# Optimization experiments

Hardware: AMD Instinct MI355X
Metric: run time of the kernel (lower is better)

Reference implementation:

```python
import jax, jax.numpy as jnp
import numpy as np
from jax import lax

B, C, L, G = 2048, 9605, 20, 50
ALPHA, ALPHA1, ALPHA2, ALPHA3, ALPHA_OTHER = 0.5, 0.05, 2.0, 10.0, 0.5
NEG_INF = jnp.float32(-1e30)


def setup_inputs() -> dict:
    k0, k1, k2, k3 = jax.random.split(jax.random.key(0), 4)
    x = jax.random.normal(k0, (B, C), jnp.float32)
    # sparse multi-label targets (~10 positives/row) so at most ~1 whitelist group is active,
    # matching the original code's assert len(gt_whitelist_index) == 1
    y = (jax.random.uniform(k1, (B, C)) < 0.001).astype(jnp.int32)
    y_neg = (jax.random.uniform(k2, (B, C)) < 0.001).astype(jnp.int32)
    # L disjoint whitelist groups of G classes each (from mapping_dict in the original)
    idx = jax.random.permutation(k3, C)[: L * G].reshape(L, G)
    group_mask = jnp.zeros((L, C), bool).at[jnp.arange(L)[:, None], idx].set(True)
    return {"x": x, "y": y, "y_neg": y_neg, "group_mask": group_mask}


def _rank_loss(x1, x2, margin):
    # our_rank_loss: sigmoid(alpha3*(x2-x1+margin)), scaled by alpha2 when positive
    d = x2 - x1 + margin
    s = jax.nn.sigmoid(ALPHA3 * d)
    return jnp.where(d > 0, ALPHA2 * s, s)


def reference(x, y, y_neg, group_mask):
    xs = jax.nn.sigmoid(x)  # [B, C]
    gmf = group_mask.astype(jnp.float32)  # [L, C]

    # per-row max score inside each whitelist group -> [B, L]
    # lax.map over the L (=20) groups keeps peak memory at one [B, C] temp per step
    group_max = lax.map(
        lambda m: jnp.max(jnp.where(m, xs, NEG_INF), axis=-1), group_mask
    ).T  # [B, L]

    # find_gt_whitelist: group k active iff sum(y[group_k]) > 0
    active = jnp.einsum("bc,lc->bl", y.astype(jnp.float32), gmf) > 0
    active_neg = jnp.einsum("bc,lc->bl", y_neg.astype(jnp.float32), gmf) > 0
    has_gt = jnp.any(active, axis=-1)  # [B]
    g = jnp.argmax(active, axis=-1)  # first active group (original asserts exactly one)

    # top_k_thres = max(11th largest sigmoid score, alpha_other) in both branches
    thres = jnp.maximum(lax.top_k(xs, 11)[0][:, 10], ALPHA_OTHER)  # [B]

    # max over union of all whitelist classes (wl_indices)
    union_max = jnp.max(jnp.where(jnp.any(group_mask, 0)[None, :], xs, NEG_INF), -1)

    gt_max = jnp.take_along_axis(group_max, g[:, None], axis=1)[:, 0]  # [B]
    # incorrect_max: max(0, max over groups != g); incorrect_neg: max(0, max over neg-active groups)
    excl = jnp.where(jnp.arange(L)[None, :] == g[:, None], NEG_INF, group_max)
    incorrect_max = jnp.maximum(jnp.max(excl, -1), 0.0)
    incorrect_neg = jnp.maximum(jnp.max(jnp.where(active_neg, group_max, 0.0), -1), 0.0)

    # branch A: no gt whitelist group active
    case_a = (1 - ALPHA) * _rank_loss(thres, union_max, ALPHA1) + ALPHA * _rank_loss(
        thres, incorrect_neg, ALPHA1
    )
    # branch B: exactly one gt group g
    case_b = (
        _rank_loss(gt_max, thres, ALPHA1)
        + jnp.where(
            incorrect_max > 0, (1 - ALPHA) * _rank_loss(thres, incorrect_max, ALPHA1), 0.0
        )
        + jnp.where(
            incorrect_neg > 0,
            ALPHA * _rank_loss(thres, incorrect_neg, ALPHA1),
            ALPHA * _rank_loss(thres, incorrect_max, ALPHA1),
        )
    )
    return jnp.sum(jnp.where(has_gt, case_b, case_a))
```

## Files before the change

### kernel.cpp

```cpp
#include <hip/hip_runtime.h>
#include <stdint.h>

#define B_ROWS 2048
#define C_CLS  9605
#define L_GRP  20
#define GM_BYTES (L_GRP * C_CLS)
#define REPSTRIDE 9728
#define NEG_BIG -3.0e38f

__device__ __forceinline__ float sigmoidf(float v) {
  return 1.0f / (1.0f + __expf(-v));
}

__device__ __forceinline__ float rank_loss(float x1, float x2) {
  float d = x2 - x1 + 0.05f;
  float s = 1.0f / (1.0f + __expf(-10.0f * d));
  return d > 0.0f ? 2.0f * s : s;
}

__device__ __forceinline__ unsigned fmap(float f) {
  unsigned u = __float_as_uint(f);
  return (u & 0x80000000u) ? ~u : (u | 0x80000000u);
}
__device__ __forceinline__ float funmap(unsigned m) {
  unsigned u = (m & 0x80000000u) ? (m ^ 0x80000000u) : ~m;
  return __uint_as_float(u);
}

__global__ void probe_init_kernel(const uint4* __restrict__ gm,
                                  unsigned char* __restrict__ ws,
                                  float* __restrict__ out,
                                  int* __restrict__ flag) {
  __shared__ int s_part[16];
  const int tid = threadIdx.x;
  if (tid == 0) out[0] = 0.0f;
  const int initbytes = 3 * REPSTRIDE + C_CLS + 16;
  for (int i = tid; i < initbytes; i += 1024) ws[64 + i] = 0xFF;
  int local = 0;
  const int nvec = GM_BYTES / 16;
  for (int i = tid; i < nvec; i += 1024) {
    uint4 w = gm[i];
    unsigned a[4] = {w.x, w.y, w.z, w.w};
#pragma unroll
    for (int q = 0; q < 4; ++q) {
      local += ((a[q] & 0x000000FFu) != 0) + ((a[q] & 0x0000FF00u) != 0) +
               ((a[q] & 0x00FF0000u) != 0) + ((a[q] & 0xFF000000u) != 0);
    }
  }
  if (tid == 0) {
    const unsigned char* gb = (const unsigned char*)gm;
    for (int i = nvec * 16; i < GM_BYTES; ++i) local += (gb[i] != 0);
  }
#pragma unroll
  for (int off = 32; off; off >>= 1) local += __shfl_xor(local, off);
  if ((tid & 63) == 0) s_part[tid >> 6] = local;
  __syncthreads();
  if (tid == 0) {
    int tot = 0;
    for (int w = 0; w < 16; ++w) tot += s_part[w];
    *flag = tot;
  }
}

__global__ void build_gid_kernel(const void* gm, const int* __restrict__ flag,
                                 unsigned char* __restrict__ ws) {
  int i = blockIdx.x * blockDim.x + threadIdx.x;
  if (i >= GM_BYTES) return;
  const bool is_byte = (*flag > 600);
  bool m;
  if (is_byte) m = ((const unsigned char*)gm)[i] != 0;
  else         m = ((const unsigned int*)gm)[i] != 0u;
  if (m) {
    int l = i / C_CLS;
    int c = i - l * C_CLS;
    unsigned char* base = ws + 64;
#pragma unroll
    for (int r = 0; r < 4; ++r) base[r * REPSTRIDE + r + c] = (unsigned char)l;
  }
}

__global__ __launch_bounds__(256, 4) void loss_kernel(
    const float* __restrict__ x, const int* __restrict__ y,
    const int* __restrict__ yn, const unsigned char* __restrict__ ws64,
    float* __restrict__ out) {
  __shared__ unsigned s_gmax[L_GRP];
  __shared__ unsigned s_act, s_actn;
  __shared__ float s_wtop[4 * 11];
  const int tid = threadIdx.x;
  const int lane = tid & 63;
  const int wave = tid >> 6;
  const int row = blockIdx.x;

  const size_t base = (size_t)row * C_CLS;
  const int mis = (int)(base & 3);
  const int peel = (4 - mis) & 3;
  const float* xr = x + base;
  const int* yr = y + base;
  const int* nr = yn + base;
  const unsigned char* gidc = ws64 + mis * REPSTRIDE + mis;

  if (tid < L_GRP) s_gmax[tid] = 0u;
  if (tid == 0) { s_act = 0u; s_actn = 0u; }
  __syncthreads();

  float t[11];
#pragma unroll
  for (int i = 0; i < 11; ++i) t[i] = 0.0f;
  unsigned actL = 0u, actnL = 0u;

  auto ins = [&](float v) {
    if (v > t[10]) {
      float a = v;
#pragma unroll
      for (int i = 0; i < 11; ++i) {
        float hi = fmaxf(t[i], a); a = fminf(t[i], a); t[i] = hi;
      }
    }
  };
  auto gmax_upd = [&](unsigned gk, float v) {
    unsigned fm = fmap(v);
    if (fm > s_gmax[gk]) atomicMax(&s_gmax[gk], fm);
  };
  auto edge = [&](int c) {
    float v = xr[c];
    ins(v);
    unsigned gk = gidc[c];
    if (gk < L_GRP) {
      gmax_upd(gk, v);
      unsigned bit = 1u << gk;
      if (yr[c] != 0) actL |= bit;
      if (nr[c] != 0) actnL |= bit;
    }
  };

  if (tid < peel) edge(tid);
  const int nvec = (C_CLS - peel) >> 2;
  const int tail0 = peel + (nvec << 2);
  if (tid < C_CLS - tail0) edge(tail0 + tid);

  const float4* x4 = (const float4*)(xr + peel);
  const int4* y4 = (const int4*)(yr + peel);
  const int4* n4 = (const int4*)(nr + peel);
  const unsigned* g4 = (const unsigned*)(gidc + peel);

  int j = tid;
  if (j < nvec) {
    float4 xa = x4[j];
    int4 ya = y4[j];
    int4 na = n4[j];
    unsigned ga = g4[j];
    for (;;) {
      const int jn = j + 256;
      const bool more = jn < nvec;
      float4 xb; int4 yb, nb; unsigned gb;
      if (more) {
        xb = x4[jn]; yb = y4[jn]; nb = n4[jn]; gb = g4[jn];
      }

      if (ga != 0xFFFFFFFFu) {
        unsigned g0 = ga & 0xFFu, g1 = (ga >> 8) & 0xFFu,
                 g2 = (ga >> 16) & 0xFFu, g3 = ga >> 24;
        if (g0 < L_GRP) gmax_upd(g0, xa.x);
        if (g1 < L_GRP) gmax_upd(g1, xa.y);
        if (g2 < L_GRP) gmax_upd(g2, xa.z);
        if (g3 < L_GRP) gmax_upd(g3, xa.w);
      }
      if (ya.x | ya.y | ya.z | ya.w | na.x | na.y | na.z | na.w) {
        const int yq[4] = {ya.x, ya.y, ya.z, ya.w};
        const int nq[4] = {na.x, na.y, na.z, na.w};
        const unsigned gq[4] = {ga & 0xFFu, (ga >> 8) & 0xFFu,
                                (ga >> 16) & 0xFFu, ga >> 24};
#pragma unroll
        for (int q = 0; q < 4; ++q) {
          if ((yq[q] | nq[q]) && gq[q] < L_GRP) {
            unsigned bit = 1u << gq[q];
            if (yq[q]) actL |= bit;
            if (nq[q]) actnL |= bit;
          }
        }
      }
      float am = fmaxf(fmaxf(xa.x, xa.y), fmaxf(xa.z, xa.w));
      if (am > t[10]) { ins(xa.x); ins(xa.y); ins(xa.z); ins(xa.w); }

      if (!more) break;
      j = jn;
      xa = xb; ya = yb; na = nb; ga = gb;
    }
  }

  if (actL) atomicOr(&s_act, actL);
  if (actnL) atomicOr(&s_actn, actnL);

  float cur = t[0];
  float mr[11];
#pragma unroll
  for (int r = 0; r < 11; ++r) {
    float m = cur;
#pragma unroll
    for (int off = 32; off; off >>= 1) m = fmaxf(m, __shfl_xor(m, off));
    mr[r] = m;
    if (r < 10) {
      unsigned long long b = __ballot(cur == m);
      int leader = (int)(__ffsll(b) - 1);
      if (lane == leader) {
#pragma unroll
        for (int i = 0; i < 10; ++i) t[i] = t[i + 1];
        t[10] = NEG_BIG;
        cur = t[0];
      }
    }
  }
  if (lane == 0) {
#pragma unroll
    for (int r = 0; r < 11; ++r) s_wtop[wave * 11 + r] = mr[r];
  }
  __syncthreads();

  if (wave == 0) {
    float v = (lane < 44) ? s_wtop[lane] : NEG_BIG;
    float eleventh = NEG_BIG;
#pragma unroll
    for (int r = 0; r < 11; ++r) {
      float m = v;
#pragma unroll
      for (int off = 32; off; off >>= 1) m = fmaxf(m, __shfl_xor(m, off));
      eleventh = m;
      if (r < 10) {
        unsigned long long b = __ballot(v == m);
        int leader = (int)(__ffsll(b) - 1);
        if (lane == leader) v = NEG_BIG;
      }
    }

    const unsigned aL = s_act, anL = s_actn;
    const bool has_gt = (aL != 0u);
    const int g = has_gt ? (__ffs(aL) - 1) : 0;
    const float thres = fmaxf(sigmoidf(eleventh), 0.5f);

    float union_max = NEG_BIG, gt_sg = 0.0f, inc_max = NEG_BIG, inc_neg = 0.0f;
#pragma unroll
    for (int l = 0; l < L_GRP; ++l) {
      float sg = sigmoidf(funmap(s_gmax[l]));
      union_max = fmaxf(union_max, sg);
      if (l == g) gt_sg = sg; else inc_max = fmaxf(inc_max, sg);
      if ((anL >> l) & 1u) inc_neg = fmaxf(inc_neg, sg);
    }
    inc_max = fmaxf(inc_max, 0.0f);
    inc_neg = fmaxf(inc_neg, 0.0f);

    float loss;
    if (has_gt) {
      loss = rank_loss(gt_sg, thres);
      if (inc_max > 0.0f) loss += 0.5f * rank_loss(thres, inc_max);
      loss += 0.5f * rank_loss(thres, (inc_neg > 0.0f) ? inc_neg : inc_max);
    } else {
      loss = 0.5f * rank_loss(thres, union_max) + 0.5f * rank_loss(thres, inc_neg);
    }
    if (lane == 0) atomicAdd(out, loss);
  }
}

extern "C" void kernel_launch(void* const* d_in, const int* in_sizes, int n_in,
                              void* d_out, int out_size, void* d_ws, size_t ws_size,
                              hipStream_t stream) {
  (void)in_sizes; (void)n_in; (void)out_size; (void)ws_size;
  const float* x = (const float*)d_in[0];
  const int* y = (const int*)d_in[1];
  const int* yn = (const int*)d_in[2];
  const void* gm = d_in[3];

  int* flag = (int*)d_ws;
  unsigned char* ws = (unsigned char*)d_ws;
  unsigned char* ws64 = ws + 64;

  probe_init_kernel<<<1, 1024, 0, stream>>>((const uint4*)gm, ws,
                                            (float*)d_out, flag);
  build_gid_kernel<<<(GM_BYTES + 255) / 256, 256, 0, stream>>>(gm, flag, ws);
  loss_kernel<<<B_ROWS, 256, 0, stream>>>(x, y, yn, ws64, (float*)d_out);
}
```

Before: 258.4 us.

## Drop software prefetch, write per-row partials, add separate reduce kernel

Replaces the manual double-buffered loads in the main scan loop with a plain strided loop, leaving latency hiding to occupancy and the compiler. Replaces the per-block atomicAdd into the output with a per-row partial store, followed by a new single-block reduction kernel. Also widens the workspace fill to 16-byte stores over the full gid region. The extra kernel launch adds a small fixed cost but makes the final sum deterministic, and dropping the prefetch may expose more memory latency.

```diff
diff --git a/kernel.cpp b/kernel.cpp
--- a/kernel.cpp
+++ b/kernel.cpp
@@ -6,6 +6,8 @@
 #define L_GRP  20
 #define GM_BYTES (L_GRP * C_CLS)
 #define REPSTRIDE 9728
+#define GID_REGION (4 * REPSTRIDE)
+#define PARTIAL_OFF (64 + GID_REGION)
 #define NEG_BIG -3.0e38f
 
 __device__ __forceinline__ float sigmoidf(float v) {
@@ -34,8 +36,10 @@
   __shared__ int s_part[16];
   const int tid = threadIdx.x;
   if (tid == 0) out[0] = 0.0f;
-  const int initbytes = 3 * REPSTRIDE + C_CLS + 16;
-  for (int i = tid; i < initbytes; i += 1024) ws[64 + i] = 0xFF;
+  uint4* gfill = (uint4*)(ws + 64);
+  const unsigned F = 0xFFFFFFFFu;
+  for (int i = tid; i < GID_REGION / 16; i += 1024)
+    gfill[i] = make_uint4(F, F, F, F);
   int local = 0;
   const int nvec = GM_BYTES / 16;
   for (int i = tid; i < nvec; i += 1024) {
@@ -82,7 +86,7 @@
 __global__ __launch_bounds__(256, 4) void loss_kernel(
     const float* __restrict__ x, const int* __restrict__ y,
     const int* __restrict__ yn, const unsigned char* __restrict__ ws64,
-    float* __restrict__ out) {
+    float* __restrict__ partial) {
   __shared__ unsigned s_gmax[L_GRP];
   __shared__ unsigned s_act, s_actn;
   __shared__ float s_wtop[4 * 11];
@@ -143,49 +147,36 @@
   const int4* n4 = (const int4*)(nr + peel);
   const unsigned* g4 = (const unsigned*)(gidc + peel);
 
-  int j = tid;
-  if (j < nvec) {
-    float4 xa = x4[j];
-    int4 ya = y4[j];
-    int4 na = n4[j];
-    unsigned ga = g4[j];
-    for (;;) {
-      const int jn = j + 256;
-      const bool more = jn < nvec;
-      float4 xb; int4 yb, nb; unsigned gb;
-      if (more) {
-        xb = x4[jn]; yb = y4[jn]; nb = n4[jn]; gb = g4[jn];
-      }
-
-      if (ga != 0xFFFFFFFFu) {
-        unsigned g0 = ga & 0xFFu, g1 = (ga >> 8) & 0xFFu,
-                 g2 = (ga >> 16) & 0xFFu, g3 = ga >> 24;
-        if (g0 < L_GRP) gmax_upd(g0, xa.x);
-        if (g1 < L_GRP) gmax_upd(g1, xa.y);
-        if (g2 < L_GRP) gmax_upd(g2, xa.z);
-        if (g3 < L_GRP) gmax_upd(g3, xa.w);
-      }
-      if (ya.x | ya.y | ya.z | ya.w | na.x | na.y | na.z | na.w) {
-        const int yq[4] = {ya.x, ya.y, ya.z, ya.w};
-        const int nq[4] = {na.x, na.y, na.z, na.w};
-        const unsigned gq[4] = {ga & 0xFFu, (ga >> 8) & 0xFFu,
-                                (ga >> 16) & 0xFFu, ga >> 24};
-#pragma unroll
-        for (int q = 0; q < 4; ++q) {
-          if ((yq[q] | nq[q]) && gq[q] < L_GRP) {
-            unsigned bit = 1u << gq[q];
-            if (yq[q]) actL |= bit;
-            if (nq[q]) actnL |= bit;
-          }
+  for (int j = tid; j < nvec; j += 256) {
+    float4 xv = x4[j];
+    int4 yv = y4[j];
+    int4 nv = n4[j];
+    unsigned gw = g4[j];
+
+    if (gw != 0xFFFFFFFFu) {
+      unsigned g0 = gw & 0xFFu, g1 = (gw >> 8) & 0xFFu,
+               g2 = (gw >> 16) & 0xFFu, g3 = gw >> 24;
+      if (g0 < L_GRP) gmax_upd(g0, xv.x);
+      if (g1 < L_GRP) gmax_upd(g1, xv.y);
+      if (g2 < L_GRP) gmax_upd(g2, xv.z);
+      if (g3 < L_GRP) gmax_upd(g3, xv.w);
+    }
+    if (yv.x | yv.y | yv.z | yv.w | nv.x | nv.y | nv.z | nv.w) {
+      const int yq[4] = {yv.x, yv.y, yv.z, yv.w};
+      const int nq[4] = {nv.x, nv.y, nv.z, nv.w};
+      const unsigned gq[4] = {gw & 0xFFu, (gw >> 8) & 0xFFu,
+                              (gw >> 16) & 0xFFu, gw >> 24};
+#pragma unroll
+      for (int q = 0; q < 4; ++q) {
+        if ((yq[q] | nq[q]) && gq[q] < L_GRP) {
+          unsigned bit = 1u << gq[q];
+          if (yq[q]) actL |= bit;
+          if (nq[q]) actnL |= bit;
         }
       }
-      float am = fmaxf(fmaxf(xa.x, xa.y), fmaxf(xa.z, xa.w));
-      if (am > t[10]) { ins(xa.x); ins(xa.y); ins(xa.z); ins(xa.w); }
-
-      if (!more) break;
-      j = jn;
-      xa = xb; ya = yb; na = nb; ga = gb;
-    }
+    }
+    float am = fmaxf(fmaxf(xv.x, xv.y), fmaxf(xv.z, xv.w));
+    if (am > t[10]) { ins(xv.x); ins(xv.y); ins(xv.z); ins(xv.w); }
   }
 
   if (actL) atomicOr(&s_act, actL);
@@ -256,8 +247,22 @@
     } else {
       loss = 0.5f * rank_loss(thres, union_max) + 0.5f * rank_loss(thres, inc_neg);
     }
-    if (lane == 0) atomicAdd(out, loss);
-  }
+    if (lane == 0) partial[row] = loss;
+  }
+}
+
+__global__ void reduce_kernel(const float* __restrict__ partial,
+                              float* __restrict__ out) {
+  __shared__ float s_p[4];
+  const int tid = threadIdx.x;
+  float v = 0.0f;
+#pragma unroll
+  for (int k = 0; k < B_ROWS / 256; ++k) v += partial[tid + k * 256];
+#pragma unroll
+  for (int off = 32; off; off >>= 1) v += __shfl_xor(v, off);
+  if ((tid & 63) == 0) s_p[tid >> 6] = v;
+  __syncthreads();
+  if (tid == 0) out[0] = s_p[0] + s_p[1] + s_p[2] + s_p[3];
 }
 
 extern "C" void kernel_launch(void* const* d_in, const int* in_sizes, int n_in,
@@ -272,9 +277,11 @@
   int* flag = (int*)d_ws;
   unsigned char* ws = (unsigned char*)d_ws;
   unsigned char* ws64 = ws + 64;
+  float* partial = (float*)(ws + PARTIAL_OFF);
 
   probe_init_kernel<<<1, 1024, 0, stream>>>((const uint4*)gm, ws,
                                             (float*)d_out, flag);
   build_gid_kernel<<<(GM_BYTES + 255) / 256, 256, 0, stream>>>(gm, flag, ws);
-  loss_kernel<<<B_ROWS, 256, 0, stream>>>(x, y, yn, ws64, (float*)d_out);
-}
+  loss_kernel<<<B_ROWS, 256, 0, stream>>>(x, y, yn, ws64, partial);
+  reduce_kernel<<<1, 256, 0, stream>>>(partial, (float*)d_out);
+}
```

New measurement: 256.2 us. Within noise of the previous version (-0.8%).
